# Optimization experiments

Hardware: AMD Instinct MI355X
Metric: run time of the kernel (lower is better)

The kernel has to match this reference:

```python
import jax, jax.numpy as jnp
import numpy as np

B, T, D, H = 4, 1024, 512, 8
DH = D // H
MLP = 4 * D
EPS = 1e-6


def _clinear(xr, xi, Wr, Wi, br, bi):
    # Naive complex Linear = two real nn.Linear layers (each adds its own bias):
    # re = Lr(xr) - Li(xi), im = Lr(xi) + Li(xr)
    re = xr @ Wr.T - xi @ Wi.T + (br - bi)
    im = xi @ Wr.T + xr @ Wi.T + (br + bi)
    return re, im


def _cln(xr, xi):
    # NaiveComplexLayerNorm: real LayerNorm (no affine) on re and im separately
    def ln(v):
        m = jnp.mean(v, -1, keepdims=True)
        va = jnp.var(v, -1, keepdims=True)
        return (v - m) * jax.lax.rsqrt(va + EPS)
    return ln(xr), ln(xi)


def _modulate(xr, xi, shr, shi, scr, sci):
    # complex x * (1 + scale) + shift, scale/shift are [B,D] broadcast over seq
    a, b = (1.0 + scr)[:, None, :], sci[:, None, :]
    return xr * a - xi * b + shr[:, None, :], xr * b + xi * a + shi[:, None, :]


def _gate(gr, gi, xr, xi):
    a, b = gr[:, None, :], gi[:, None, :]
    return xr * a - xi * b, xr * b + xi * a


def _heads(x):  # [B,T,D] -> [B,H,T,DH]
    return x.reshape(B, T, H, DH).transpose(0, 2, 1, 3)


def reference(x_re, x_im, c_re, c_im,
              ada_Wr, ada_Wi, ada_br, ada_bi,
              q_Wr, q_Wi, q_br, q_bi,
              k_Wr, k_Wi, k_br, k_bi,
              v_Wr, v_Wi, v_br, v_bi,
              o_Wr, o_Wi, o_br, o_bi,
              f1_Wr, f1_Wi, f1_br, f1_bi,
              f2_Wr, f2_Wi, f2_br, f2_bi):
    # adaLN_modulation: complex SiLU -> complex Linear -> 6 chunks along dim 1
    sr, si = jax.nn.silu(c_re), jax.nn.silu(c_im)
    mr, mi = _clinear(sr, si, ada_Wr, ada_Wi, ada_br, ada_bi)
    sh_ar, sc_ar, g_ar, sh_mr, sc_mr, g_mr = jnp.split(mr, 6, axis=1)
    sh_ai, sc_ai, g_ai, sh_mi, sc_mi, g_mi = jnp.split(mi, 6, axis=1)

    nr, ni = _cln(x_re, x_im)
    hr, hi = _modulate(nr, ni, sh_ar, sh_ai, sc_ar, sc_ai)

    qr, qi = _clinear(hr, hi, q_Wr, q_Wi, q_br, q_bi)
    kr, ki = _clinear(hr, hi, k_Wr, k_Wi, k_br, k_bi)
    vr, vi = _clinear(hr, hi, v_Wr, v_Wi, v_br, v_bi)
    qr, qi, kr, ki, vr, vi = map(_heads, (qr, qi, kr, ki, vr, vi))

    scale = 1.0 / jnp.sqrt(jnp.float32(DH))
    # complex scores q @ k^T (no conjugation, matching plain complex matmul)
    s_re = (jnp.einsum('bhqd,bhkd->bhqk', qr, kr) - jnp.einsum('bhqd,bhkd->bhqk', qi, ki)) * scale
    s_im = (jnp.einsum('bhqd,bhkd->bhqk', qr, ki) + jnp.einsum('bhqd,bhkd->bhqk', qi, kr)) * scale
    # naive complex softmax: real softmax applied to re/im independently
    a_re = jax.nn.softmax(s_re, axis=-1)
    a_im = jax.nn.softmax(s_im, axis=-1)
    o_r = jnp.einsum('bhqk,bhkd->bhqd', a_re, vr) - jnp.einsum('bhqk,bhkd->bhqd', a_im, vi)
    o_i = jnp.einsum('bhqk,bhkd->bhqd', a_re, vi) + jnp.einsum('bhqk,bhkd->bhqd', a_im, vr)
    o_r = o_r.transpose(0, 2, 1, 3).reshape(B, T, D)
    o_i = o_i.transpose(0, 2, 1, 3).reshape(B, T, D)
    o_r, o_i = _clinear(o_r, o_i, o_Wr, o_Wi, o_br, o_bi)

    gr, gi = _gate(g_ar, g_ai, o_r, o_i)
    x_re, x_im = x_re + gr, x_im + gi

    # ---- MLP branch
    nr, ni = _cln(x_re, x_im)
    hr, hi = _modulate(nr, ni, sh_mr, sh_mi, sc_mr, sc_mi)
    hr, hi = _clinear(hr, hi, f1_Wr, f1_Wi, f1_br, f1_bi)
    hr = jax.nn.gelu(hr, approximate=True)  # ComplexGELU(tanh) per component
    hi = jax.nn.gelu(hi, approximate=True)
    hr, hi = _clinear(hr, hi, f2_Wr, f2_Wi, f2_br, f2_bi)
    gr, gi = _gate(g_mr, g_mi, hr, hi)
    return jnp.stack([x_re + gr, x_im + gi])  # [2,B,T,D] = (real, imag)


def setup_inputs() -> dict:
    key = jax.random.key(0)
    ks = iter(jax.random.split(key, 48))

    def rn(shape, s=1.0):
        return jax.random.normal(next(ks), shape, dtype=jnp.float32) * s

    inp = {'x_re': rn((B, T, D)), 'x_im': rn((B, T, D)),
           'c_re': rn((B, D)), 'c_im': rn((B, D))}

    def lin(name, din, dout):
        inp[name + '_Wr'] = rn((dout, din), 0.02)
        inp[name + '_Wi'] = rn((dout, din), 0.02)
        inp[name + '_br'] = rn((dout,), 0.02)
        inp[name + '_bi'] = rn((dout,), 0.02)

    lin('ada', D, 6 * D)
    for n in ('q', 'k', 'v', 'o'):
        lin(n, D, D)
    lin('f1', D, MLP)
    lin('f2', MLP, D)
    return inp
```

## Files before the change

### kernel.cpp

```cpp
#include <hip/hip_runtime.h>


typedef unsigned short u16;
typedef __attribute__((ext_vector_type(8))) __bf16 bf16x8;
typedef __attribute__((ext_vector_type(8))) u16    u16x8;
typedef __attribute__((ext_vector_type(4))) u16    u16x4;
typedef __attribute__((ext_vector_type(4))) float  f32x4;

#define MFMA16(a, b, c) __builtin_amdgcn_mfma_f32_16x16x32_bf16(a, b, c, 0, 0, 0)

static constexpr int Bd = 4, Td = 1024, Dd = 512, Hd = 8, DHd = 64, MLPd = 2048;

__device__ __forceinline__ u16 f2bf(float x) {
  return __builtin_bit_cast(u16, (__bf16)x);
}
__device__ __forceinline__ float exp2fast(float x) {
  return __builtin_amdgcn_exp2f(x);
}
__device__ __forceinline__ bf16x8 ldsfrag(const u16* p) {
  return __builtin_bit_cast(bf16x8, *(const u16x8*)p);
}
__device__ __forceinline__ bf16x8 gfrag(const u16* p) {
  return __builtin_bit_cast(bf16x8, *(const u16x8*)p);
}
__device__ __forceinline__ bf16x8 negbf(bf16x8 v) {
  u16x8 u = __builtin_bit_cast(u16x8, v);
  u ^= (u16)0x8000;
  return __builtin_bit_cast(bf16x8, u);
}
__device__ __forceinline__ float gelu_tanh(float x) {
  float t = tanhf(0.7978845608028654f * (x + 0.044715f * x * x * x));
  return 0.5f * x * (1.f + t);
}

template <int CTRL>
__device__ __forceinline__ float dppror(float x) {
  const int xi = __builtin_bit_cast(int, x);
  return __builtin_bit_cast(float,
      __builtin_amdgcn_update_dpp(xi, xi, CTRL, 0xf, 0xf, false));
}
__device__ __forceinline__ float red16max(float x) {
  x = fmaxf(x, dppror<0x128>(x));
  x = fmaxf(x, dppror<0x124>(x));
  x = fmaxf(x, dppror<0x122>(x));
  x = fmaxf(x, dppror<0x121>(x));
  return x;
}
__device__ __forceinline__ float red16sum(float x) {
  x += dppror<0x128>(x);
  x += dppror<0x124>(x);
  x += dppror<0x122>(x);
  x += dppror<0x121>(x);
  return x;
}

struct CJobs {
  const float* src[12];
  u16* dst[12];
  int blk_start[13];
};
__global__ __launch_bounds__(256) void convert_kernel(CJobs J) {
  const int blk = blockIdx.x;
  int jj = 0;
  while (jj < 11 && blk >= J.blk_start[jj + 1]) ++jj;
  const int idx = (blk - J.blk_start[jj]) * 256 + threadIdx.x;
  const float4 v = ((const float4*)J.src[jj])[idx];
  u16x4 o;
  o[0] = f2bf(v.x); o[1] = f2bf(v.y); o[2] = f2bf(v.z); o[3] = f2bf(v.w);
  *(u16x4*)(J.dst[jj] + (size_t)idx * 4) = o;
}

__global__ __launch_bounds__(256) void ada_kernel(
    const float* __restrict__ c_re, const float* __restrict__ c_im,
    const float* __restrict__ Wr, const float* __restrict__ Wi,
    const float* __restrict__ br, const float* __restrict__ bi,
    float* __restrict__ m_r, float* __restrict__ m_i) {
  __shared__ __align__(16) float sr[512], si[512];
  const int b = blockIdx.x / 12, nb = blockIdx.x % 12;
  const int tid = threadIdx.x;
  for (int i = tid; i < 512; i += 256) {
    const float xr = c_re[b * 512 + i], xi = c_im[b * 512 + i];
    sr[i] = xr / (1.f + __expf(-xr));
    si[i] = xi / (1.f + __expf(-xi));
  }
  __syncthreads();
  const int n = nb * 256 + tid;
  const float4* wr4 = (const float4*)(Wr + (size_t)n * 512);
  const float4* wi4 = (const float4*)(Wi + (size_t)n * 512);
  const float4* sr4 = (const float4*)sr;
  const float4* si4 = (const float4*)si;
  float ar = 0.f, ai = 0.f;
  for (int k = 0; k < 128; ++k) {
    const float4 a_ = sr4[k], b_ = si4[k], u = wr4[k], v = wi4[k];
    ar += a_.x * u.x - b_.x * v.x + a_.y * u.y - b_.y * v.y +
          a_.z * u.z - b_.z * v.z + a_.w * u.w - b_.w * v.w;
    ai += b_.x * u.x + a_.x * v.x + b_.y * u.y + a_.y * v.y +
          b_.z * u.z + a_.z * v.z + b_.w * u.w + a_.w * v.w;
  }
  m_r[(size_t)b * 3072 + n] = ar + br[n] - bi[n];
  m_i[(size_t)b * 3072 + n] = ai + br[n] + bi[n];
}

__global__ __launch_bounds__(256) void ln_mod_kernel(
    const float* __restrict__ xr, const float* __restrict__ xi,
    const float* __restrict__ mv_r, const float* __restrict__ mv_i,
    int off_sh, int off_sc,
    u16* __restrict__ hr, u16* __restrict__ hi) {
  const int row = blockIdx.x;
  const int b = row >> 10;
  const int tid = threadIdx.x;
  const float* xrp = xr + (size_t)row * 512;
  const float* xip = xi + (size_t)row * 512;
  const float r0 = xrp[tid], r1 = xrp[tid + 256];
  const float i0 = xip[tid], i1 = xip[tid + 256];
  float s0 = r0 + r1, s1 = r0 * r0 + r1 * r1;
  float s2 = i0 + i1, s3 = i0 * i0 + i1 * i1;
  #pragma unroll
  for (int o = 32; o > 0; o >>= 1) {
    s0 += __shfl_down(s0, o); s1 += __shfl_down(s1, o);
    s2 += __shfl_down(s2, o); s3 += __shfl_down(s3, o);
  }
  __shared__ float red[4][4];
  if ((tid & 63) == 0) {
    const int wv = tid >> 6;
    red[wv][0] = s0; red[wv][1] = s1; red[wv][2] = s2; red[wv][3] = s3;
  }
  __syncthreads();
  s0 = red[0][0] + red[1][0] + red[2][0] + red[3][0];
  s1 = red[0][1] + red[1][1] + red[2][1] + red[3][1];
  s2 = red[0][2] + red[1][2] + red[2][2] + red[3][2];
  s3 = red[0][3] + red[1][3] + red[2][3] + red[3][3];
  const float mr = s0 * (1.f / 512.f), mi = s2 * (1.f / 512.f);
  const float vr = s1 * (1.f / 512.f) - mr * mr;
  const float vi = s3 * (1.f / 512.f) - mi * mi;
  const float rr = rsqrtf(vr + 1e-6f), ri = rsqrtf(vi + 1e-6f);
  const float* shr = mv_r + (size_t)b * 3072 + off_sh;
  const float* shi = mv_i + (size_t)b * 3072 + off_sh;
  const float* scr = mv_r + (size_t)b * 3072 + off_sc;
  const float* sci = mv_i + (size_t)b * 3072 + off_sc;
  #pragma unroll
  for (int jj = 0; jj < 2; ++jj) {
    const int n = tid + jj * 256;
    const float nr = ((jj ? r1 : r0) - mr) * rr;
    const float ni = ((jj ? i1 : i0) - mi) * ri;
    const float a = 1.f + scr[n], bb = sci[n];
    hr[(size_t)row * 512 + n] = f2bf(nr * a - ni * bb + shr[n]);
    hi[(size_t)row * 512 + n] = f2bf(nr * bb + ni * a + shi[n]);
  }
}

template <int EPI>
__global__ __launch_bounds__(256) void cgemm_kernel(
    const u16* __restrict__ Ar, const u16* __restrict__ Ai,
    const u16* __restrict__ W0r, const u16* __restrict__ W0i,
    const float* __restrict__ b0r, const float* __restrict__ b0i,
    const u16* __restrict__ W1r, const u16* __restrict__ W1i,
    const float* __restrict__ b1r, const float* __restrict__ b1i,
    const u16* __restrict__ W2r, const u16* __restrict__ W2i,
    const float* __restrict__ b2r, const float* __restrict__ b2i,
    int K, int ntiles_per_seg, int out_ld,
    u16* __restrict__ o0r, u16* __restrict__ o0i,
    u16* __restrict__ o1r, u16* __restrict__ o1i,
    u16* __restrict__ o2r, u16* __restrict__ o2i,
    const float* __restrict__ resid_r, const float* __restrict__ resid_i,
    const float* __restrict__ gate_r, const float* __restrict__ gate_i,
    float* __restrict__ ofr, float* __restrict__ ofi) {
  const int seg = blockIdx.y / ntiles_per_seg;
  const int n0 = (blockIdx.y % ntiles_per_seg) * 64;
  const int m0 = blockIdx.x * 64;
  const u16* Wr = (seg == 0) ? W0r : (seg == 1) ? W1r : W2r;
  const u16* Wi = (seg == 0) ? W0i : (seg == 1) ? W1i : W2i;
  const float* br = (seg == 0) ? b0r : (seg == 1) ? b1r : b2r;
  const float* bi = (seg == 0) ? b0i : (seg == 1) ? b1i : b2i;
  u16* obr = (seg == 0) ? o0r : (seg == 1) ? o1r : o2r;
  u16* obi = (seg == 0) ? o0i : (seg == 1) ? o1i : o2i;

  __shared__ __align__(16) u16 sA[2][64 * 72];
  __shared__ __align__(16) u16 sB[2][64 * 72];

  const int tid = threadIdx.x;
  const int w = tid >> 6, lane = tid & 63;
  const int wm = w >> 1, wn = w & 1;
  const int q4 = lane >> 4, c = lane & 15;

  const f32x4 z = {0.f, 0.f, 0.f, 0.f};
  f32x4 accR[2][2], accI[2][2];
  for (int a = 0; a < 2; ++a)
    for (int b2 = 0; b2 < 2; ++b2) { accR[a][b2] = z; accI[a][b2] = z; }

  for (int kt = 0; kt < K; kt += 64) {
    for (int idx = tid; idx < 512; idx += 256) {
      const int row = idx >> 3, cg = idx & 7;
      const int lo = row * 72 + cg * 8;
      *(u16x8*)&sA[0][lo] = *(const u16x8*)(Ar + (size_t)(m0 + row) * K + kt + cg * 8);
      *(u16x8*)&sA[1][lo] = *(const u16x8*)(Ai + (size_t)(m0 + row) * K + kt + cg * 8);
      *(u16x8*)&sB[0][lo] = *(const u16x8*)(Wr + (size_t)(n0 + row) * K + kt + cg * 8);
      *(u16x8*)&sB[1][lo] = *(const u16x8*)(Wi + (size_t)(n0 + row) * K + kt + cg * 8);
    }
    __syncthreads();
    #pragma unroll
    for (int kc = 0; kc < 2; ++kc) {
      bf16x8 a_r[2], a_i[2], a_n[2];
      #pragma unroll
      for (int mi = 0; mi < 2; ++mi) {
        const int off = (wm * 32 + mi * 16 + c) * 72 + kc * 32 + q4 * 8;
        a_r[mi] = ldsfrag(&sA[0][off]);
        a_i[mi] = ldsfrag(&sA[1][off]);
        a_n[mi] = negbf(a_i[mi]);
      }
      #pragma unroll
      for (int ni = 0; ni < 2; ++ni) {
        const int off = (wn * 32 + ni * 16 + c) * 72 + kc * 32 + q4 * 8;
        const bf16x8 b_r = ldsfrag(&sB[0][off]);
        const bf16x8 b_i = ldsfrag(&sB[1][off]);
        #pragma unroll
        for (int mi = 0; mi < 2; ++mi) {
          accR[mi][ni] = MFMA16(a_r[mi], b_r, accR[mi][ni]);
          accR[mi][ni] = MFMA16(a_n[mi], b_i, accR[mi][ni]);
          accI[mi][ni] = MFMA16(a_i[mi], b_r, accI[mi][ni]);
          accI[mi][ni] = MFMA16(a_r[mi], b_i, accI[mi][ni]);
        }
      }
    }
    __syncthreads();
  }

  const float scale = (EPI == 0 && seg == 0) ? 0.18033688011112042f : 1.f;
  #pragma unroll
  for (int mi = 0; mi < 2; ++mi)
    #pragma unroll
    for (int ni = 0; ni < 2; ++ni) {
      const int n = n0 + wn * 32 + ni * 16 + c;
      const float biasr = br[n] - bi[n];
      const float biasi = br[n] + bi[n];
      if (EPI == 0 && seg == 2) {
        const int m = m0 + wm * 32 + mi * 16 + q4 * 4;
        u16x4 pr, pi;
        #pragma unroll
        for (int r = 0; r < 4; ++r) {
          pr[r] = f2bf(accR[mi][ni][r] + biasr);
          pi[r] = f2bf(accI[mi][ni][r] + biasi);
        }
        const size_t o = ((size_t)((m >> 10) * 512 + n)) * 1024 + (m & 1023);
        *(u16x4*)(obr + o) = pr;
        *(u16x4*)(obi + o) = pi;
        continue;
      }
      #pragma unroll
      for (int r = 0; r < 4; ++r) {
        const int m = m0 + wm * 32 + mi * 16 + q4 * 4 + r;
        const float ore = accR[mi][ni][r] + biasr;
        const float oim = accI[mi][ni][r] + biasi;
        if (EPI == 0) {
          obr[(size_t)m * out_ld + n] = f2bf(ore * scale);
          obi[(size_t)m * out_ld + n] = f2bf(oim * scale);
        } else if (EPI == 2) {
          obr[(size_t)m * out_ld + n] = f2bf(gelu_tanh(ore));
          obi[(size_t)m * out_ld + n] = f2bf(gelu_tanh(oim));
        } else {
          const int bb = m >> 10;
          const float gr = gate_r[(size_t)bb * 3072 + n];
          const float gi = gate_i[(size_t)bb * 3072 + n];
          const size_t o = (size_t)m * 512 + n;
          ofr[o] = resid_r[o] + ore * gr - oim * gi;
          ofi[o] = resid_i[o] + ore * gi + oim * gr;
        }
      }
    }
}

__global__ __launch_bounds__(256, 2) void attn_kernel(
    const u16* __restrict__ Qr, const u16* __restrict__ Qi,
    const u16* __restrict__ Kr, const u16* __restrict__ Ki,
    const u16* __restrict__ Vtr, const u16* __restrict__ Vti,
    u16* __restrict__ Or, u16* __restrict__ Oi) {
  __shared__ __align__(16) u16 sP[2][4][16 * 72];

  const int tid = threadIdx.x;
  const int w = tid >> 6, lane = tid & 63;
  const int q4 = lane >> 4, c = lane & 15;
  const int bh = blockIdx.y, b = bh >> 3, h = bh & 7;
  const int t0 = blockIdx.x * 64;
  const size_t base = (size_t)b * Td * Dd + h * DHd;
  const size_t vbase = (size_t)bh << 16;

  bf16x8 aQr[2], aQi[2], aQn[2];
  #pragma unroll
  for (int kc = 0; kc < 2; ++kc) {
    const size_t g = base + (size_t)(t0 + w * 16 + c) * Dd + kc * 32 + q4 * 8;
    aQr[kc] = gfrag(Qr + g);
    aQi[kc] = gfrag(Qi + g);
    aQn[kc] = negbf(aQi[kc]);
  }

  float mst[2][4], lst[2][4];
  #pragma unroll
  for (int p = 0; p < 2; ++p)
    for (int r = 0; r < 4; ++r) { mst[p][r] = -1e30f; lst[p][r] = 0.f; }
  const f32x4 z = {0.f, 0.f, 0.f, 0.f};
  f32x4 U1[4], U2[4], U3[4], U4[4];
  for (int i = 0; i < 4; ++i) { U1[i] = z; U2[i] = z; U3[i] = z; U4[i] = z; }

  u16* const pR = &sP[0][w][0];
  u16* const pI = &sP[1][w][0];

  for (int kt = 0; kt < 16; ++kt) {
    bf16x8 kR[4][2], kI[4][2];
    #pragma unroll
    for (int nb = 0; nb < 4; ++nb)
      #pragma unroll
      for (int kc = 0; kc < 2; ++kc) {
        const size_t g = base + (size_t)(kt * 64 + nb * 16 + c) * Dd + kc * 32 + q4 * 8;
        kR[nb][kc] = gfrag(Kr + g);
        kI[nb][kc] = gfrag(Ki + g);
      }

    f32x4 S[2][4];
    __builtin_amdgcn_s_setprio(1);
    #pragma unroll
    for (int nb = 0; nb < 4; ++nb) {
      f32x4 tr = z, ti = z;
      #pragma unroll
      for (int kc = 0; kc < 2; ++kc) {
        tr = MFMA16(aQr[kc], kR[nb][kc], tr);
        tr = MFMA16(aQn[kc], kI[nb][kc], tr);
        ti = MFMA16(aQi[kc], kR[nb][kc], ti);
        ti = MFMA16(aQr[kc], kI[nb][kc], ti);
      }
      S[0][nb] = tr; S[1][nb] = ti;
    }
    __builtin_amdgcn_s_setprio(0);

    bf16x8 vR[4][2], vI[4][2];
    #pragma unroll
    for (int nd = 0; nd < 4; ++nd)
      #pragma unroll
      for (int kc = 0; kc < 2; ++kc) {
        const size_t gv = vbase + (size_t)(nd * 16 + c) * Td + kt * 64 + kc * 32 + q4 * 8;
        vR[nd][kc] = gfrag(Vtr + gv);
        vI[nd][kc] = gfrag(Vti + gv);
      }

    float alpha[2][4];
    #pragma unroll
    for (int p = 0; p < 2; ++p) {
      u16* const pp = (p == 0) ? pR : pI;
      float rs[4];
      #pragma unroll
      for (int r = 0; r < 4; ++r) {
        float tm = fmaxf(fmaxf(S[p][0][r], S[p][1][r]), fmaxf(S[p][2][r], S[p][3][r]));
        tm = red16max(tm);
        const float mn = fmaxf(mst[p][r], tm);
        alpha[p][r] = exp2fast(mst[p][r] - mn);
        mst[p][r] = mn;
        rs[r] = 0.f;
      }
      #pragma unroll
      for (int nb = 0; nb < 4; ++nb)
        #pragma unroll
        for (int r = 0; r < 4; ++r) {
          const float pv = exp2fast(S[p][nb][r] - mst[p][r]);
          rs[r] += pv;
          pp[(q4 * 4 + r) * 72 + nb * 16 + c] = f2bf(pv);
        }
      #pragma unroll
      for (int r = 0; r < 4; ++r)
        lst[p][r] = lst[p][r] * alpha[p][r] + red16sum(rs[r]);
    }
    #pragma unroll
    for (int i = 0; i < 4; ++i)
      #pragma unroll
      for (int r = 0; r < 4; ++r) {
        U1[i][r] *= alpha[0][r]; U2[i][r] *= alpha[0][r];
        U3[i][r] *= alpha[1][r]; U4[i][r] *= alpha[1][r];
      }

    asm volatile("s_waitcnt lgkmcnt(0)" ::: "memory");
    __builtin_amdgcn_s_setprio(1);
    #pragma unroll
    for (int kc = 0; kc < 2; ++kc) {
      const int poff = c * 72 + kc * 32 + q4 * 8;
      const bf16x8 aPr = ldsfrag(pR + poff);
      const bf16x8 aPi = ldsfrag(pI + poff);
      #pragma unroll
      for (int nd = 0; nd < 4; ++nd) {
        U1[nd] = MFMA16(aPr, vR[nd][kc], U1[nd]);
        U2[nd] = MFMA16(aPr, vI[nd][kc], U2[nd]);
        U3[nd] = MFMA16(aPi, vR[nd][kc], U3[nd]);
        U4[nd] = MFMA16(aPi, vI[nd][kc], U4[nd]);
      }
    }
    __builtin_amdgcn_s_setprio(0);
  }

  #pragma unroll
  for (int nd = 0; nd < 4; ++nd)
    #pragma unroll
    for (int r = 0; r < 4; ++r) {
      const int trow = t0 + w * 16 + q4 * 4 + r;
      const int d = nd * 16 + c;
      const float ilre = 1.f / lst[0][r], ilim = 1.f / lst[1][r];
      const float ore = U1[nd][r] * ilre - U4[nd][r] * ilim;
      const float oim = U2[nd][r] * ilre + U3[nd][r] * ilim;
      const size_t g = base + (size_t)trow * Dd + d;
      Or[g] = f2bf(ore);
      Oi[g] = f2bf(oim);
    }
}

extern "C" void kernel_launch(void* const* d_in, const int* in_sizes, int n_in,
                              void* d_out, int out_size, void* d_ws, size_t ws_size,
                              hipStream_t stream) {
  const float* x_re  = (const float*)d_in[0];
  const float* x_im  = (const float*)d_in[1];
  const float* c_re  = (const float*)d_in[2];
  const float* c_im  = (const float*)d_in[3];
  const float* adaWr = (const float*)d_in[4];
  const float* adaWi = (const float*)d_in[5];
  const float* adabr = (const float*)d_in[6];
  const float* adabi = (const float*)d_in[7];
  const float* qWr = (const float*)d_in[8],  *qWi = (const float*)d_in[9];
  const float* qbr = (const float*)d_in[10], *qbi = (const float*)d_in[11];
  const float* kWr = (const float*)d_in[12], *kWi = (const float*)d_in[13];
  const float* kbr = (const float*)d_in[14], *kbi = (const float*)d_in[15];
  const float* vWr = (const float*)d_in[16], *vWi = (const float*)d_in[17];
  const float* vbr = (const float*)d_in[18], *vbi = (const float*)d_in[19];
  const float* oWr = (const float*)d_in[20], *oWi = (const float*)d_in[21];
  const float* obr = (const float*)d_in[22], *obi = (const float*)d_in[23];
  const float* f1Wr = (const float*)d_in[24], *f1Wi = (const float*)d_in[25];
  const float* f1br = (const float*)d_in[26], *f1bi = (const float*)d_in[27];
  const float* f2Wr = (const float*)d_in[28], *f2Wi = (const float*)d_in[29];
  const float* f2br = (const float*)d_in[30], *f2bi = (const float*)d_in[31];

  char* wsp = (char*)d_ws;
  size_t off = 0;
  auto alloc = [&](size_t bytes) -> void* {
    void* p = wsp + off;
    off += (bytes + 255) & ~(size_t)255;
    return p;
  };
  const size_t WQ = 512 * 512, WF = 2048 * 512;
  u16* wqr = (u16*)alloc(WQ * 2); u16* wqi = (u16*)alloc(WQ * 2);
  u16* wkr = (u16*)alloc(WQ * 2); u16* wki = (u16*)alloc(WQ * 2);
  u16* wvr = (u16*)alloc(WQ * 2); u16* wvi = (u16*)alloc(WQ * 2);
  u16* wor = (u16*)alloc(WQ * 2); u16* woi = (u16*)alloc(WQ * 2);
  u16* wf1r = (u16*)alloc(WF * 2); u16* wf1i = (u16*)alloc(WF * 2);
  u16* wf2r = (u16*)alloc(WF * 2); u16* wf2i = (u16*)alloc(WF * 2);
  float* m_r = (float*)alloc(4 * 3072 * 4);
  float* m_i = (float*)alloc(4 * 3072 * 4);
  const size_t ACT = (size_t)Bd * Td * Dd;
  u16* h1r = (u16*)alloc(ACT * 2); u16* h1i = (u16*)alloc(ACT * 2);
  u16* qbr_ = (u16*)alloc(ACT * 2); u16* qbi_ = (u16*)alloc(ACT * 2);
  u16* kbr_ = (u16*)alloc(ACT * 2); u16* kbi_ = (u16*)alloc(ACT * 2);
  u16* vbr_ = (u16*)alloc(ACT * 2); u16* vbi_ = (u16*)alloc(ACT * 2);
  u16* atr = (u16*)alloc(ACT * 2); u16* ati = (u16*)alloc(ACT * 2);
  float* x2r = (float*)alloc(ACT * 4); float* x2i = (float*)alloc(ACT * 4);
  u16* h2r = h1r; u16* h2i = h1i;
  u16* f1or = qbr_;
  u16* f1oi = qbr_ + (size_t)Bd * Td * MLPd;

  CJobs J;
  const float* wsrc[12] = {qWr, qWi, kWr, kWi, vWr, vWi, oWr, oWi, f1Wr, f1Wi, f2Wr, f2Wi};
  u16* wdst[12] = {wqr, wqi, wkr, wki, wvr, wvi, wor, woi, wf1r, wf1i, wf2r, wf2i};
  int cum = 0;
  for (int j = 0; j < 12; ++j) {
    J.src[j] = wsrc[j]; J.dst[j] = wdst[j]; J.blk_start[j] = cum;
    cum += (j < 8 ? (int)WQ : (int)WF) / 1024;
  }
  J.blk_start[12] = cum;
  convert_kernel<<<cum, 256, 0, stream>>>(J);

  ada_kernel<<<48, 256, 0, stream>>>(c_re, c_im, adaWr, adaWi, adabr, adabi, m_r, m_i);

  ln_mod_kernel<<<4096, 256, 0, stream>>>(x_re, x_im, m_r, m_i, 0, 512, h1r, h1i);

  cgemm_kernel<0><<<dim3(64, 24), 256, 0, stream>>>(
      h1r, h1i, wqr, wqi, qbr, qbi, wkr, wki, kbr, kbi, wvr, wvi, vbr, vbi,
      512, 8, 512, qbr_, qbi_, kbr_, kbi_, vbr_, vbi_,
      nullptr, nullptr, nullptr, nullptr, nullptr, nullptr);

  attn_kernel<<<dim3(16, 32), 256, 0, stream>>>(qbr_, qbi_, kbr_, kbi_, vbr_, vbi_, atr, ati);

  cgemm_kernel<1><<<dim3(64, 8), 256, 0, stream>>>(
      atr, ati, wor, woi, obr, obi, wor, woi, obr, obi, wor, woi, obr, obi,
      512, 8, 512, nullptr, nullptr, nullptr, nullptr, nullptr, nullptr,
      x_re, x_im, m_r + 1024, m_i + 1024, x2r, x2i);

  ln_mod_kernel<<<4096, 256, 0, stream>>>(x2r, x2i, m_r, m_i, 1536, 2048, h2r, h2i);

  cgemm_kernel<2><<<dim3(64, 32), 256, 0, stream>>>(
      h2r, h2i, wf1r, wf1i, f1br, f1bi, wf1r, wf1i, f1br, f1bi, wf1r, wf1i, f1br, f1bi,
      512, 32, 2048, f1or, f1oi, nullptr, nullptr, nullptr, nullptr,
      nullptr, nullptr, nullptr, nullptr, nullptr, nullptr);

  float* outp = (float*)d_out;
  cgemm_kernel<3><<<dim3(64, 8), 256, 0, stream>>>(
      f1or, f1oi, wf2r, wf2i, f2br, f2bi, wf2r, wf2i, f2br, f2bi, wf2r, wf2i, f2br, f2bi,
      2048, 8, 512, nullptr, nullptr, nullptr, nullptr, nullptr, nullptr,
      x2r, x2i, m_r + 2560, m_i + 2560, outp, outp + ACT);
}
```

Baseline: 478.0 us.

## Stage GEMM and attention K/V tiles via global_load_lds into XOR-swizzled LDS

Replaces register-staged global-to-LDS copies in the complex GEMM with direct global_load_lds transfers into an unpadded, XOR-swizzled 64-wide LDS layout, adjusting fragment reads to match. In the attention kernel, K and V tiles were previously read straight from global memory into registers by each wave. They are now double-buffered in shared memory through global_load_lds, with the next tile prefetched while the current one is computed. This cuts redundant per-wave global loads and register pressure, but adds LDS use (about 64KB more per block, which may lower occupancy) and relies on the hardware's load-to-LDS semantics and the vmcnt/barrier ordering being correct.

```diff
diff --git a/kernel.cpp b/kernel.cpp
--- a/kernel.cpp
+++ b/kernel.cpp
@@ -31,6 +31,11 @@
 __device__ __forceinline__ float gelu_tanh(float x) {
   float t = tanhf(0.7978845608028654f * (x + 0.044715f * x * x * x));
   return 0.5f * x * (1.f + t);
+}
+__device__ __forceinline__ void gll16(const u16* g, u16* l) {
+  __builtin_amdgcn_global_load_lds(
+      (const __attribute__((address_space(1))) unsigned int*)g,
+      (__attribute__((address_space(3))) unsigned int*)l, 16, 0, 0);
 }
 
 template <int CTRL>
@@ -175,13 +180,15 @@
   u16* obr = (seg == 0) ? o0r : (seg == 1) ? o1r : o2r;
   u16* obi = (seg == 0) ? o0i : (seg == 1) ? o1i : o2i;
 
-  __shared__ __align__(16) u16 sA[2][64 * 72];
-  __shared__ __align__(16) u16 sB[2][64 * 72];
+  __shared__ __align__(16) u16 sA[2][64 * 64];
+  __shared__ __align__(16) u16 sB[2][64 * 64];
 
   const int tid = threadIdx.x;
   const int w = tid >> 6, lane = tid & 63;
   const int wm = w >> 1, wn = w & 1;
   const int q4 = lane >> 4, c = lane & 15;
+  const int r8 = lane >> 3, jsw = (lane & 7) ^ r8;
+  const int c7 = c & 7;
 
   const f32x4 z = {0.f, 0.f, 0.f, 0.f};
   f32x4 accR[2][2], accI[2][2];
@@ -189,13 +196,15 @@
     for (int b2 = 0; b2 < 2; ++b2) { accR[a][b2] = z; accI[a][b2] = z; }
 
   for (int kt = 0; kt < K; kt += 64) {
-    for (int idx = tid; idx < 512; idx += 256) {
-      const int row = idx >> 3, cg = idx & 7;
-      const int lo = row * 72 + cg * 8;
-      *(u16x8*)&sA[0][lo] = *(const u16x8*)(Ar + (size_t)(m0 + row) * K + kt + cg * 8);
-      *(u16x8*)&sA[1][lo] = *(const u16x8*)(Ai + (size_t)(m0 + row) * K + kt + cg * 8);
-      *(u16x8*)&sB[0][lo] = *(const u16x8*)(Wr + (size_t)(n0 + row) * K + kt + cg * 8);
-      *(u16x8*)&sB[1][lo] = *(const u16x8*)(Wi + (size_t)(n0 + row) * K + kt + cg * 8);
+    #pragma unroll
+    for (int half = 0; half < 2; ++half) {
+      const int rr = w * 16 + half * 8;
+      const size_t ga = (size_t)(m0 + rr + r8) * K + kt + jsw * 8;
+      gll16(Ar + ga, &sA[0][rr * 64]);
+      gll16(Ai + ga, &sA[1][rr * 64]);
+      const size_t gb = (size_t)(n0 + rr + r8) * K + kt + jsw * 8;
+      gll16(Wr + gb, &sB[0][rr * 64]);
+      gll16(Wi + gb, &sB[1][rr * 64]);
     }
     __syncthreads();
     #pragma unroll
@@ -203,14 +212,14 @@
       bf16x8 a_r[2], a_i[2], a_n[2];
       #pragma unroll
       for (int mi = 0; mi < 2; ++mi) {
-        const int off = (wm * 32 + mi * 16 + c) * 72 + kc * 32 + q4 * 8;
+        const int off = (wm * 32 + mi * 16 + c) * 64 + (((kc * 4 + q4) ^ c7) * 8);
         a_r[mi] = ldsfrag(&sA[0][off]);
         a_i[mi] = ldsfrag(&sA[1][off]);
         a_n[mi] = negbf(a_i[mi]);
       }
       #pragma unroll
       for (int ni = 0; ni < 2; ++ni) {
-        const int off = (wn * 32 + ni * 16 + c) * 72 + kc * 32 + q4 * 8;
+        const int off = (wn * 32 + ni * 16 + c) * 64 + (((kc * 4 + q4) ^ c7) * 8);
         const bf16x8 b_r = ldsfrag(&sB[0][off]);
         const bf16x8 b_i = ldsfrag(&sB[1][off]);
         #pragma unroll
@@ -274,15 +283,19 @@
     const u16* __restrict__ Kr, const u16* __restrict__ Ki,
     const u16* __restrict__ Vtr, const u16* __restrict__ Vti,
     u16* __restrict__ Or, u16* __restrict__ Oi) {
+  __shared__ __align__(16) u16 sK[2][2][64 * 64];
+  __shared__ __align__(16) u16 sV[2][2][64 * 64];
   __shared__ __align__(16) u16 sP[2][4][16 * 72];
 
   const int tid = threadIdx.x;
   const int w = tid >> 6, lane = tid & 63;
   const int q4 = lane >> 4, c = lane & 15;
+  const int c7 = c & 7;
   const int bh = blockIdx.y, b = bh >> 3, h = bh & 7;
   const int t0 = blockIdx.x * 64;
   const size_t base = (size_t)b * Td * Dd + h * DHd;
   const size_t vbase = (size_t)bh << 16;
+  const int r8 = lane >> 3, jsw = (lane & 7) ^ r8;
 
   bf16x8 aQr[2], aQi[2], aQn[2];
   #pragma unroll
@@ -304,16 +317,25 @@
   u16* const pR = &sP[0][w][0];
   u16* const pI = &sP[1][w][0];
 
+  auto stage = [&](int kt, int bi) {
+    #pragma unroll
+    for (int half = 0; half < 2; ++half) {
+      const int rr = w * 16 + half * 8;
+      const size_t gk = base + (size_t)(kt * 64 + rr + r8) * Dd + jsw * 8;
+      gll16(Kr + gk, &sK[bi][0][rr * 64]);
+      gll16(Ki + gk, &sK[bi][1][rr * 64]);
+      const size_t gv = vbase + (size_t)(rr + r8) * Td + kt * 64 + jsw * 8;
+      gll16(Vtr + gv, &sV[bi][0][rr * 64]);
+      gll16(Vti + gv, &sV[bi][1][rr * 64]);
+    }
+  };
+
+  stage(0, 0);
+
   for (int kt = 0; kt < 16; ++kt) {
-    bf16x8 kR[4][2], kI[4][2];
-    #pragma unroll
-    for (int nb = 0; nb < 4; ++nb)
-      #pragma unroll
-      for (int kc = 0; kc < 2; ++kc) {
-        const size_t g = base + (size_t)(kt * 64 + nb * 16 + c) * Dd + kc * 32 + q4 * 8;
-        kR[nb][kc] = gfrag(Kr + g);
-        kI[nb][kc] = gfrag(Ki + g);
-      }
+    __syncthreads();
+    if (kt < 15) stage(kt + 1, (kt + 1) & 1);
+    const int bi = kt & 1;
 
     f32x4 S[2][4];
     __builtin_amdgcn_s_setprio(1);
@@ -322,24 +344,17 @@
       f32x4 tr = z, ti = z;
       #pragma unroll
       for (int kc = 0; kc < 2; ++kc) {
-        tr = MFMA16(aQr[kc], kR[nb][kc], tr);
-        tr = MFMA16(aQn[kc], kI[nb][kc], tr);
-        ti = MFMA16(aQi[kc], kR[nb][kc], ti);
-        ti = MFMA16(aQr[kc], kI[nb][kc], ti);
+        const int off = (nb * 16 + c) * 64 + (((kc * 4 + q4) ^ c7) * 8);
+        const bf16x8 bKr = ldsfrag(&sK[bi][0][off]);
+        const bf16x8 bKi = ldsfrag(&sK[bi][1][off]);
+        tr = MFMA16(aQr[kc], bKr, tr);
+        tr = MFMA16(aQn[kc], bKi, tr);
+        ti = MFMA16(aQi[kc], bKr, ti);
+        ti = MFMA16(aQr[kc], bKi, ti);
       }
       S[0][nb] = tr; S[1][nb] = ti;
     }
     __builtin_amdgcn_s_setprio(0);
-
-    bf16x8 vR[4][2], vI[4][2];
-    #pragma unroll
-    for (int nd = 0; nd < 4; ++nd)
-      #pragma unroll
-      for (int kc = 0; kc < 2; ++kc) {
-        const size_t gv = vbase + (size_t)(nd * 16 + c) * Td + kt * 64 + kc * 32 + q4 * 8;
-        vR[nd][kc] = gfrag(Vtr + gv);
-        vI[nd][kc] = gfrag(Vti + gv);
-      }
 
     float alpha[2][4];
     #pragma unroll
@@ -384,10 +399,13 @@
       const bf16x8 aPi = ldsfrag(pI + poff);
       #pragma unroll
       for (int nd = 0; nd < 4; ++nd) {
-        U1[nd] = MFMA16(aPr, vR[nd][kc], U1[nd]);
-        U2[nd] = MFMA16(aPr, vI[nd][kc], U2[nd]);
-        U3[nd] = MFMA16(aPi, vR[nd][kc], U3[nd]);
-        U4[nd] = MFMA16(aPi, vI[nd][kc], U4[nd]);
+        const int voff = (nd * 16 + c) * 64 + (((kc * 4 + q4) ^ c7) * 8);
+        const bf16x8 bVr = ldsfrag(&sV[bi][0][voff]);
+        const bf16x8 bVi = ldsfrag(&sV[bi][1][voff]);
+        U1[nd] = MFMA16(aPr, bVr, U1[nd]);
+        U2[nd] = MFMA16(aPr, bVi, U2[nd]);
+        U3[nd] = MFMA16(aPi, bVr, U3[nd]);
+        U4[nd] = MFMA16(aPi, bVi, U4[nd]);
       }
     }
     __builtin_amdgcn_s_setprio(0);
```

Measured after the change: 427.9 us. 10.5% less time.
